# Kernel optimization log

Measured on AMD Instinct MI355X. Metric: run time of the kernel, lower is better.

The kernel has to match this reference:

```python
import jax, jax.numpy as jnp
import numpy as np

D = 256
H = 4
L = 6
N = 32768
NH = N // H  # 8192 per-head width
VOCAB = 256
B, T = 1, 1024
ROPE_BASE = 10000.0


def ln(x):
    # LayerNorm over last dim, no affine (elementwise_affine=False)
    m = jnp.mean(x, axis=-1, keepdims=True)
    v = jnp.var(x, axis=-1, keepdims=True)
    return (x - m) * jax.lax.rsqrt(v + 1e-5)


def rope(x):
    # standard rotary position embedding over the last dim (split-half convention)
    Dh = x.shape[-1]
    t = x.shape[-2]
    half = Dh // 2
    inv_freq = 1.0 / (ROPE_BASE ** (jnp.arange(half, dtype=jnp.float32) / half))
    ang = jnp.arange(t, dtype=jnp.float32)[:, None] * inv_freq[None, :]  # [T, half]
    cos, sin = jnp.cos(ang), jnp.sin(ang)
    x1, x2 = x[..., :half], x[..., half:]
    return jnp.concatenate([x1 * cos - x2 * sin, x2 * cos + x1 * sin], axis=-1)


def setup_inputs() -> dict:
    key = jax.random.key(0)
    ks = jax.random.split(key, 6)
    std = 0.02
    return {
        "idx": jax.random.randint(ks[0], (B, T), 0, VOCAB, dtype=jnp.int32),
        "wte": std * jax.random.normal(ks[1], (VOCAB, D), dtype=jnp.float32),
        "encoder": std * jax.random.normal(ks[2], (N, D), dtype=jnp.float32),
        "decoder_x": std * jax.random.normal(ks[3], (H, D, NH), dtype=jnp.float32),
        "decoder_y": std * jax.random.normal(ks[4], (H, D, NH), dtype=jnp.float32),
        "readout": std * jax.random.normal(ks[5], (D, VOCAB), dtype=jnp.float32),
    }


def reference(idx, wte, encoder, decoder_x, decoder_y, readout):
    b, t = idx.shape
    v = ln(wte[idx])  # [B, T, D]
    # strict causal mask (tril with diagonal=-1): position i attends to j < i
    mask = jnp.tril(jnp.ones((t, t), dtype=bool), k=-1)
    for _ in range(L):
        # x: relu(v @ decoder_x) -> [B, H, T, NH]
        x = jax.nn.relu(jnp.einsum('btd,hdn->bhtn', v, decoder_x))
        xr = rope(x)  # Q = K = x
        # unnormalized causal linear attention, strict lower triangular
        scores = jnp.einsum('bhtn,bhsn->bhts', xr, xr)
        scores = jnp.where(mask, scores, 0.0)
        a = jnp.einsum('bhts,bsd->bhtd', scores, v)  # V = v (broadcast over heads)
        # gated wide projection
        y = jax.nn.relu(jnp.einsum('bhtd,hdn->bhtn', ln(a), decoder_y)) * x
        # [B,H,T,NH] -> [B,T,H*NH] = [B,T,N]  (matches transpose(1,2).reshape)
        y = jnp.transpose(y, (0, 2, 1, 3)).reshape(b, t, N)
        v = ln(v + ln(y @ encoder))  # dropout is identity in eval
    return v @ readout  # [B, T, VOCAB]
```

## Files before the change

### kernel.cpp

```cpp
#include <hip/hip_runtime.h>
#include <hip/hip_bf16.h>
#include <stdint.h>

typedef unsigned short u16;
typedef unsigned int u32;
typedef __attribute__((ext_vector_type(8))) short i16x8;
typedef __attribute__((ext_vector_type(4))) float f32x4;

#define DEV __device__ __forceinline__

constexpr int T = 1024, D = 256, H = 4, NH = 8192, NF = 32768, HALF = 4096;

constexpr size_t OFF_DXT  = 0;
constexpr size_t OFF_DYT  = OFF_DXT  + (size_t)H*NH*D*2;
constexpr size_t OFF_ENCT = OFF_DYT  + (size_t)H*NH*D*2;
constexpr size_t OFF_ROT  = OFF_ENCT + (size_t)D*NF*2;
constexpr size_t OFF_COS  = OFF_ROT  + (size_t)D*D*2;
constexpr size_t OFF_SIN  = OFF_COS  + (size_t)T*HALF*4;
constexpr size_t OFF_V    = OFF_SIN  + (size_t)T*HALF*4;
constexpr size_t OFF_VBF  = OFF_V    + (size_t)T*D*4;
constexpr size_t OFF_VT   = OFF_VBF  + (size_t)T*D*2;
constexpr size_t OFF_X    = OFF_VT   + (size_t)T*D*2;
constexpr size_t OFF_XR   = OFF_X    + (size_t)T*NF*2;
constexpr size_t OFF_SC   = OFF_XR   + (size_t)T*NF*2;
constexpr size_t OFF_LA   = OFF_SC   + (size_t)H*T*T*2;
constexpr size_t OFF_PART = OFF_LA   + (size_t)H*T*D*2;
constexpr size_t WS_NEED  = OFF_PART + (size_t)8*T*T*4;


DEV u16 f2bf(float f) {
  u32 u = __float_as_uint(f);
  u += 0x7FFFu + ((u >> 16) & 1u);
  return (u16)(u >> 16);
}
DEV float bf2f(u16 u) { return __uint_as_float(((u32)u) << 16); }

DEV float2 block_sum2(float a, float b, float* sb) {
  #pragma unroll
  for (int o = 32; o > 0; o >>= 1) {
    a += __shfl_down(a, o, 64);
    b += __shfl_down(b, o, 64);
  }
  const int w = threadIdx.x >> 6;
  __syncthreads();
  if ((threadIdx.x & 63) == 0) { sb[w*2] = a; sb[w*2+1] = b; }
  __syncthreads();
  return make_float2(sb[0]+sb[2]+sb[4]+sb[6], sb[1]+sb[3]+sb[5]+sb[7]);
}

DEV void stage128(const u16* __restrict__ g, int ld, char* lds, int wave, int lane) {
  #pragma unroll
  for (int i = 0; i < 4; ++i) {
    const int f = (wave*4 + i)*64 + lane;
    const int row = f >> 3, seg = f & 7;
    const int segl = seg ^ (row & 7);
    const u16* src = g + (size_t)row*ld + segl*8;
    __builtin_amdgcn_global_load_lds(
        (const __attribute__((address_space(1))) void*)src,
        (__attribute__((address_space(3))) void*)(lds + ((wave*4 + i) << 10)),
        16, 0, 0);
  }
}

DEV void mfma_tile(const char* Ac, const char* Bc, int wm, int wn, int lr, int lk,
                   f32x4 acc[4][4]) {
  #pragma unroll
  for (int kk = 0; kk < 2; ++kk) {
    const int lcol = kk*64 + lk*16;
    i16x8 af[4], bfv[4];
    #pragma unroll
    for (int m = 0; m < 4; ++m) {
      const int row = wm*64 + m*16 + lr;
      af[m] = *(const i16x8*)(Ac + row*128 + (lcol ^ ((row & 7) << 4)));
    }
    #pragma unroll
    for (int n = 0; n < 4; ++n) {
      const int row = wn*64 + n*16 + lr;
      bfv[n] = *(const i16x8*)(Bc + row*128 + (lcol ^ ((row & 7) << 4)));
    }
    #pragma unroll
    for (int m = 0; m < 4; ++m)
      #pragma unroll
      for (int n = 0; n < 4; ++n)
        acc[m][n] = __builtin_amdgcn_mfma_f32_16x16x32_bf16(af[m], bfv[n], acc[m][n], 0, 0, 0);
  }
}

DEV void gemm_bt_core(const u16* __restrict__ Ab, int lda,
                      const u16* __restrict__ Bb, int ldb,
                      int nkt, char* smem, f32x4 acc[4][4]) {
  const int tid = threadIdx.x, lane = tid & 63, wave = tid >> 6;
  const int wm = wave >> 1, wn = wave & 1;
  const int lr = lane & 15, lk = lane >> 4;
  char* As = smem;
  char* Bs = smem + 32768;
  #pragma unroll
  for (int m = 0; m < 4; ++m)
    #pragma unroll
    for (int n = 0; n < 4; ++n) acc[m][n] = f32x4{0.f, 0.f, 0.f, 0.f};
  stage128(Ab, lda, As, wave, lane);
  stage128(Bb, ldb, Bs, wave, lane);
  __syncthreads();
  for (int kt = 0; kt < nkt; ++kt) {
    const int cur = kt & 1;
    if (kt + 1 < nkt) {
      stage128(Ab + (size_t)(kt+1)*64, lda, As + ((cur^1) << 14), wave, lane);
      stage128(Bb + (size_t)(kt+1)*64, ldb, Bs + ((cur^1) << 14), wave, lane);
    }
    mfma_tile(As + (cur << 14), Bs + (cur << 14), wm, wn, lr, lk, acc);
    __syncthreads();
  }
}

DEV void gemm_bt_core_sb(const u16* __restrict__ Ab, int lda,
                         const u16* __restrict__ Bb, int ldb,
                         int nkt, char* smem, f32x4 acc[4][4]) {
  const int tid = threadIdx.x, lane = tid & 63, wave = tid >> 6;
  const int wm = wave >> 1, wn = wave & 1;
  const int lr = lane & 15, lk = lane >> 4;
  char* As = smem;
  char* Bs = smem + 16384;
  #pragma unroll
  for (int m = 0; m < 4; ++m)
    #pragma unroll
    for (int n = 0; n < 4; ++n) acc[m][n] = f32x4{0.f, 0.f, 0.f, 0.f};
  for (int kt = 0; kt < nkt; ++kt) {
    stage128(Ab + (size_t)kt*64, lda, As, wave, lane);
    stage128(Bb + (size_t)kt*64, ldb, Bs, wave, lane);
    __syncthreads();
    mfma_tile(As, Bs, wm, wn, lr, lk, acc);
    __syncthreads();
  }
}

#define EPILOG_IDX() \
  const int lane = threadIdx.x & 63, wave = threadIdx.x >> 6; \
  const int wm = wave >> 1, wn = wave & 1, lr = lane & 15, lk = lane >> 4; \
  const int r0 = wm*64 + lk*4; \
  const int c0 = wn*64 + lr;

constexpr int TS = 136;

template<int MODE>
DEV void store_tile(const f32x4 acc[4][4], u16* __restrict__ dst, int ld,
                    const u16* __restrict__ xg, char* smem) {
  u16* tb = (u16*)smem;
  EPILOG_IDX();
  #pragma unroll
  for (int m = 0; m < 4; ++m)
    #pragma unroll
    for (int n = 0; n < 4; ++n)
      #pragma unroll
      for (int r = 0; r < 4; ++r) {
        float v = acc[m][n][r];
        if (MODE >= 1) v = fmaxf(v, 0.f);
        tb[(size_t)(r0 + m*16 + r)*TS + c0 + n*16] = f2bf(v);
      }
  __syncthreads();
  const int rr = threadIdx.x >> 4;
  const int cc = (threadIdx.x & 15)*8;
  #pragma unroll
  for (int it = 0; it < 8; ++it) {
    const int row = it*16 + rr;
    i16x8 w = *(const i16x8*)(tb + (size_t)row*TS + cc);
    if (MODE == 2) {
      const i16x8 xv = *(const i16x8*)(xg + (size_t)row*ld + cc);
      #pragma unroll
      for (int j = 0; j < 8; ++j)
        w[j] = (short)f2bf(bf2f((u16)w[j]) * bf2f((u16)xv[j]));
    }
    *(i16x8*)(dst + (size_t)row*ld + cc) = w;
  }
}

template<int MODE>
DEV void store_tile_sb(const f32x4 acc[4][4], u16* __restrict__ dst, int ld,
                       const u16* __restrict__ xg, char* smem) {
  u16* tb = (u16*)smem;
  const int lane = threadIdx.x & 63, wave = threadIdx.x >> 6;
  const int wm = wave >> 1, wn = wave & 1, lr = lane & 15, lk = lane >> 4;
  const int c0 = wn*64 + lr, rb = lk*4;
  const int rr = threadIdx.x >> 4, cc = (threadIdx.x & 15)*8;
  #pragma unroll
  for (int half = 0; half < 2; ++half) {
    if (wm == half) {
      #pragma unroll
      for (int m = 0; m < 4; ++m)
        #pragma unroll
        for (int n = 0; n < 4; ++n)
          #pragma unroll
          for (int r = 0; r < 4; ++r) {
            float v = acc[m][n][r];
            if (MODE >= 1) v = fmaxf(v, 0.f);
            tb[(size_t)(rb + m*16 + r)*TS + c0 + n*16] = f2bf(v);
          }
    }
    __syncthreads();
    #pragma unroll
    for (int it = 0; it < 4; ++it) {
      const int row = it*16 + rr;
      const int grow = half*64 + row;
      i16x8 w = *(const i16x8*)(tb + (size_t)row*TS + cc);
      if (MODE == 2) {
        const i16x8 xv = *(const i16x8*)(xg + (size_t)grow*ld + cc);
        #pragma unroll
        for (int j = 0; j < 8; ++j)
          w[j] = (short)f2bf(bf2f((u16)w[j]) * bf2f((u16)xv[j]));
      }
      *(i16x8*)(dst + (size_t)grow*ld + cc) = w;
    }
    __syncthreads();
  }
}

template<int PERM>
__global__ __launch_bounds__(256) void k_transpose_cvt(const float* __restrict__ in,
                                                       u16* __restrict__ out, int R, int C) {
  __shared__ float tile[32][33];
  const size_t zoff = (size_t)blockIdx.z * R * C;
  const float* inz = in + zoff;
  u16* outz = out + zoff;
  const int c0 = blockIdx.x << 5, rr0 = blockIdx.y << 5;
  const int tx = threadIdx.x & 31, ty = threadIdx.x >> 5;
  #pragma unroll
  for (int i = 0; i < 4; ++i) {
    int irow = rr0 + ty + i*8;
    if (PERM == 2) {
      const int hh = irow >> 13, j = irow & 8191;
      irow = hh*8192 + ((j & 1) ? (j >> 1) + 4096 : (j >> 1));
    }
    tile[ty + i*8][tx] = inz[(size_t)irow*C + c0 + tx];
  }
  __syncthreads();
  #pragma unroll
  for (int i = 0; i < 4; ++i) {
    const int rr = ty + i*8;
    int orow = c0 + rr;
    if (PERM == 1) {
      const int j = orow & 8191;
      orow = (orow & ~8191) | ((j < 4096) ? 2*j : 2*(j - 4096) + 1);
    }
    outz[(size_t)orow*R + rr0 + tx] = f2bf(tile[tx][rr]);
  }
}

__global__ __launch_bounds__(256) void k_rope_table(float* __restrict__ cosT,
                                                    float* __restrict__ sinT) {
  const int i = blockIdx.x*256 + threadIdx.x;
  const int t = blockIdx.y;
  const float p = (float)i * (1.f/4096.f);
  const float ang = (float)t * expf(-9.210340371976184f * p);
  cosT[(size_t)t*HALF + i] = cosf(ang);
  sinT[(size_t)t*HALF + i] = sinf(ang);
}

__global__ __launch_bounds__(256) void k_embed(const int* __restrict__ idx,
                                               const float* __restrict__ wte,
                                               float* __restrict__ v,
                                               u16* __restrict__ vbf, u16* __restrict__ vT) {
  __shared__ float sb[8];
  const int t = blockIdx.x, d = threadIdx.x;
  const float val = wte[(size_t)idx[t]*D + d];
  float2 ss = block_sum2(val, val*val, sb);
  const float m = ss.x*(1.f/256.f), var = ss.y*(1.f/256.f) - m*m;
  const float vn = (val - m) * rsqrtf(var + 1e-5f);
  v[(size_t)t*D + d] = vn;
  const u16 b = f2bf(vn);
  vbf[(size_t)t*D + d] = b;
  vT[(size_t)d*T + t] = b;
}

__global__ __launch_bounds__(256) void k_gemm_x_rope(const u16* __restrict__ vbf,
                                                     const u16* __restrict__ dxT,
                                                     u16* __restrict__ x,
                                                     u16* __restrict__ xr,
                                                     const float* __restrict__ cosT,
                                                     const float* __restrict__ sinT) {
  __shared__ char smem[32768];
  const int nt = blockIdx.x, mt = blockIdx.y, h = blockIdx.z;
  f32x4 acc[4][4];
  gemm_bt_core_sb(vbf + (size_t)mt*128*D, D,
                  dxT + ((size_t)h*NH + (size_t)nt*128)*D, D, 4, smem, acc);
  u16* tb = (u16*)smem;
  const int lane = threadIdx.x & 63, wave = threadIdx.x >> 6;
  const int wm = wave >> 1, wn = wave & 1, lr = lane & 15, lk = lane >> 4;
  const int c0 = wn*64 + lr, rb = lk*4;
  const int rr = threadIdx.x >> 4, cc = (threadIdx.x & 15)*8;
  const size_t obase = (size_t)mt*128*NF + (size_t)h*NH + (size_t)nt*128;
  const int pbase = (nt*128 + cc) >> 1;
  #pragma unroll
  for (int half = 0; half < 2; ++half) {
    if (wm == half) {
      #pragma unroll
      for (int m = 0; m < 4; ++m)
        #pragma unroll
        for (int n = 0; n < 4; ++n)
          #pragma unroll
          for (int r = 0; r < 4; ++r)
            tb[(size_t)(rb + m*16 + r)*TS + c0 + n*16] = f2bf(fmaxf(acc[m][n][r], 0.f));
    }
    __syncthreads();
    #pragma unroll
    for (int it = 0; it < 4; ++it) {
      const int row = it*16 + rr;
      const int grow = half*64 + row;
      const i16x8 w = *(const i16x8*)(tb + (size_t)row*TS + cc);
      *(i16x8*)(x + obase + (size_t)grow*NF + cc) = w;
      const int t = mt*128 + grow;
      const float4 cv = *(const float4*)(cosT + (size_t)t*HALF + pbase);
      const float4 sv = *(const float4*)(sinT + (size_t)t*HALF + pbase);
      i16x8 rg;
      float x1, x2;
      x1 = bf2f((u16)w[0]); x2 = bf2f((u16)w[1]);
      rg[0] = (short)f2bf(x1*cv.x - x2*sv.x); rg[1] = (short)f2bf(x2*cv.x + x1*sv.x);
      x1 = bf2f((u16)w[2]); x2 = bf2f((u16)w[3]);
      rg[2] = (short)f2bf(x1*cv.y - x2*sv.y); rg[3] = (short)f2bf(x2*cv.y + x1*sv.y);
      x1 = bf2f((u16)w[4]); x2 = bf2f((u16)w[5]);
      rg[4] = (short)f2bf(x1*cv.z - x2*sv.z); rg[5] = (short)f2bf(x2*cv.z + x1*sv.z);
      x1 = bf2f((u16)w[6]); x2 = bf2f((u16)w[7]);
      rg[6] = (short)f2bf(x1*cv.w - x2*sv.w); rg[7] = (short)f2bf(x2*cv.w + x1*sv.w);
      *(i16x8*)(xr + obase + (size_t)grow*NF + cc) = rg;
    }
    __syncthreads();
  }
}

__global__ __launch_bounds__(256) void k_gemm_sc(const u16* __restrict__ xr,
                                                 u16* __restrict__ scb) {
  __shared__ char smem[65536];
  const int z = blockIdx.x & 15;
  const int i = blockIdx.x >> 4;
  int tt = 0;
  while ((tt + 1)*(tt + 2)/2 <= i) ++tt;
  const int st = i - tt*(tt + 1)/2;
  const int h = z >> 2, kc = z & 3;
  const u16* base = xr + (size_t)h*NH + (size_t)kc*2048;
  f32x4 acc[4][4];
  gemm_bt_core(base + (size_t)tt*128*NF, NF, base + (size_t)st*128*NF, NF, 32, smem, acc);
  store_tile<0>(acc, scb + (size_t)z*T*T + (size_t)tt*128*T + (size_t)st*128, T,
                nullptr, smem);
}

__global__ __launch_bounds__(256) void k_sc_combine(const u16* __restrict__ scb,
                                                    u16* __restrict__ sc) {
  const int row = blockIdx.x;
  const int h = row >> 10, t = row & 1023;
  const u16* p0 = scb + ((size_t)(h*4 + 0)*T + t)*T;
  u16* o = sc + (size_t)row*T;
  const int s0 = threadIdx.x*4;
  ushort4 r;
  if (s0 >= t) {
    r.x = 0; r.y = 0; r.z = 0; r.w = 0;
  } else {
    const ushort4 a0 = *(const ushort4*)(p0 + s0);
    const ushort4 a1 = *(const ushort4*)(p0 + T*T + s0);
    const ushort4 a2 = *(const ushort4*)(p0 + 2*(size_t)T*T + s0);
    const ushort4 a3 = *(const ushort4*)(p0 + 3*(size_t)T*T + s0);
    const float vx = bf2f(a0.x) + bf2f(a1.x) + bf2f(a2.x) + bf2f(a3.x);
    const float vy = bf2f(a0.y) + bf2f(a1.y) + bf2f(a2.y) + bf2f(a3.y);
    const float vz = bf2f(a0.z) + bf2f(a1.z) + bf2f(a2.z) + bf2f(a3.z);
    const float vw = bf2f(a0.w) + bf2f(a1.w) + bf2f(a2.w) + bf2f(a3.w);
    r.x = f2bf((s0 + 0 < t) ? vx : 0.f);
    r.y = f2bf((s0 + 1 < t) ? vy : 0.f);
    r.z = f2bf((s0 + 2 < t) ? vz : 0.f);
    r.w = f2bf((s0 + 3 < t) ? vw : 0.f);
  }
  *(ushort4*)(o + s0) = r;
}

__global__ __launch_bounds__(256) void k_gemm_av(const u16* __restrict__ sc,
                                                 const u16* __restrict__ vT,
                                                 float* __restrict__ part) {
  __shared__ char smem[65536];
  const int slot = blockIdx.x & 7;
  const int h = slot >> 1, nt = slot & 1;
  int mt = 0, kc = 0, rem = blockIdx.x >> 3;
  #pragma unroll
  for (int m = 0; m < 8; ++m) {
    const int c = (m >> 1) + 1;
    if (rem < c) { mt = m; kc = rem; break; }
    rem -= c;
  }
  f32x4 acc[4][4];
  gemm_bt_core(sc + ((size_t)h*T + (size_t)mt*128)*T + (size_t)kc*256, T,
               vT + (size_t)nt*128*T + (size_t)kc*256, T, 4, smem, acc);
  EPILOG_IDX();
  float* Cp = part + (size_t)(h*4 + kc) * T * D;
  const int tb = mt*128 + r0, cb = nt*128 + c0;
  #pragma unroll
  for (int m = 0; m < 4; ++m)
    #pragma unroll
    for (int n = 0; n < 4; ++n)
      #pragma unroll
      for (int r = 0; r < 4; ++r)
        Cp[(size_t)(tb + m*16 + r)*D + cb + n*16] = acc[m][n][r];
}

__global__ __launch_bounds__(256) void k_ln_a(const float* __restrict__ part,
                                              u16* __restrict__ la) {
  __shared__ float sb[8];
  const int row = blockIdx.x;
  const int h = row >> 10, t = row & 1023;
  const int d = threadIdx.x;
  const int nkc = ((t >> 7) >> 1) + 1;
  float s = 0.f;
  for (int kc = 0; kc < nkc; ++kc)
    s += part[((size_t)(h*4 + kc)*T + t)*D + d];
  float2 ss = block_sum2(s, s*s, sb);
  const float m = ss.x*(1.f/256.f), var = ss.y*(1.f/256.f) - m*m;
  la[(size_t)row*D + d] = f2bf((s - m) * rsqrtf(var + 1e-5f));
}

__global__ __launch_bounds__(256) void k_gemm_y(const u16* __restrict__ la,
                                                const u16* __restrict__ dyT,
                                                const u16* __restrict__ x,
                                                u16* __restrict__ y) {
  __shared__ char smem[32768];
  const int nt = blockIdx.x, mt = blockIdx.y, h = blockIdx.z;
  f32x4 acc[4][4];
  gemm_bt_core_sb(la + ((size_t)h*T + (size_t)mt*128)*D, D,
                  dyT + ((size_t)h*NH + (size_t)nt*128)*D, D, 4, smem, acc);
  const size_t off = (size_t)mt*128*NF + (size_t)h*NH + (size_t)nt*128;
  store_tile_sb<2>(acc, y + off, NF, x + off, smem);
}

__global__ __launch_bounds__(256) void k_gemm_enc(const u16* __restrict__ y,
                                                  const u16* __restrict__ encT,
                                                  float* __restrict__ part) {
  __shared__ char smem[65536];
  const int slot = blockIdx.x & 7;
  const int seq  = blockIdx.x >> 3;
  const int kcc = slot*4 + (seq >> 4);
  const int nt = seq & 1;
  const int mt = (seq >> 1) & 7;
  f32x4 acc[4][4];
  gemm_bt_core(y + (size_t)mt*128*NF + (size_t)kcc*1024, NF,
               encT + (size_t)nt*128*NF + (size_t)kcc*1024, NF, 16, smem, acc);
  EPILOG_IDX();
  float* Cp = part + (size_t)kcc * T * D;
  const int tb = mt*128 + r0, cb = nt*128 + c0;
  #pragma unroll
  for (int m = 0; m < 4; ++m)
    #pragma unroll
    for (int n = 0; n < 4; ++n)
      #pragma unroll
      for (int r = 0; r < 4; ++r)
        Cp[(size_t)(tb + m*16 + r)*D + cb + n*16] = acc[m][n][r];
}

__global__ __launch_bounds__(256) void k_newv(const float* __restrict__ part,
                                              float* __restrict__ v,
                                              u16* __restrict__ vbf, u16* __restrict__ vT) {
  __shared__ float sb[8];
  const int t = blockIdx.x, d = threadIdx.x;
  float s = 0.f;
  #pragma unroll
  for (int kc = 0; kc < 32; ++kc)
    s += part[((size_t)kc*T + t)*D + d];
  float2 ss = block_sum2(s, s*s, sb);
  float m = ss.x*(1.f/256.f), var = ss.y*(1.f/256.f) - m*m;
  const float l1 = (s - m) * rsqrtf(var + 1e-5f);
  const float u = v[(size_t)t*D + d] + l1;
  float2 s2 = block_sum2(u, u*u, sb);
  m = s2.x*(1.f/256.f); var = s2.y*(1.f/256.f) - m*m;
  const float vn = (u - m) * rsqrtf(var + 1e-5f);
  v[(size_t)t*D + d] = vn;
  const u16 bb = f2bf(vn);
  vbf[(size_t)t*D + d] = bb;
  vT[(size_t)d*T + t] = bb;
}

__global__ __launch_bounds__(256) void k_gemm_out(const u16* __restrict__ vbf,
                                                  const u16* __restrict__ roT,
                                                  float* __restrict__ out) {
  __shared__ char smem[65536];
  const int nt = blockIdx.x, mt = blockIdx.y;
  f32x4 acc[4][4];
  gemm_bt_core(vbf + (size_t)mt*128*D, D, roT + (size_t)nt*128*D, D, 4, smem, acc);
  EPILOG_IDX();
  const int tb = mt*128 + r0, cb = nt*128 + c0;
  #pragma unroll
  for (int m = 0; m < 4; ++m)
    #pragma unroll
    for (int n = 0; n < 4; ++n)
      #pragma unroll
      for (int r = 0; r < 4; ++r)
        out[(size_t)(tb + m*16 + r)*D + cb + n*16] = acc[m][n][r];
}

extern "C" void kernel_launch(void* const* d_in, const int* in_sizes, int n_in,
                              void* d_out, int out_size, void* d_ws, size_t ws_size,
                              hipStream_t stream) {
  (void)in_sizes; (void)n_in; (void)out_size; (void)ws_size;
  const int*   idx = (const int*)d_in[0];
  const float* wte = (const float*)d_in[1];
  const float* enc = (const float*)d_in[2];
  const float* dx  = (const float*)d_in[3];
  const float* dy  = (const float*)d_in[4];
  const float* ro  = (const float*)d_in[5];
  float* out = (float*)d_out;
  char* ws = (char*)d_ws;

  u16* dxT  = (u16*)(ws + OFF_DXT);
  u16* dyT  = (u16*)(ws + OFF_DYT);
  u16* encT = (u16*)(ws + OFF_ENCT);
  u16* roT  = (u16*)(ws + OFF_ROT);
  float* cosT = (float*)(ws + OFF_COS);
  float* sinT = (float*)(ws + OFF_SIN);
  float* v    = (float*)(ws + OFF_V);
  u16* vbf  = (u16*)(ws + OFF_VBF);
  u16* vT   = (u16*)(ws + OFF_VT);
  u16* x    = (u16*)(ws + OFF_X);
  u16* xr   = (u16*)(ws + OFF_XR);
  u16* sc   = (u16*)(ws + OFF_SC);
  u16* la   = (u16*)(ws + OFF_LA);
  u16* scb  = (u16*)(ws + OFF_PART);
  float* part = (float*)(ws + OFF_PART);

  k_transpose_cvt<1><<<dim3(NH/32, D/32, H), 256, 0, stream>>>(dx, dxT, D, NH);
  k_transpose_cvt<1><<<dim3(NH/32, D/32, H), 256, 0, stream>>>(dy, dyT, D, NH);
  k_transpose_cvt<2><<<dim3(D/32, NF/32, 1), 256, 0, stream>>>(enc, encT, NF, D);
  k_transpose_cvt<0><<<dim3(D/32, D/32, 1), 256, 0, stream>>>(ro, roT, D, D);
  k_rope_table<<<dim3(HALF/256, T), 256, 0, stream>>>(cosT, sinT);
  k_embed<<<T, 256, 0, stream>>>(idx, wte, v, vbf, vT);

  for (int l = 0; l < 6; ++l) {
    k_gemm_x_rope<<<dim3(64, 8, H), 256, 0, stream>>>(vbf, dxT, x, xr, cosT, sinT);
    k_gemm_sc <<<576,              256, 0, stream>>>(xr, scb);
    k_sc_combine<<<H*T,            256, 0, stream>>>(scb, sc);
    k_gemm_av <<<160,              256, 0, stream>>>(sc, vT, part);
    k_ln_a    <<<H*T,              256, 0, stream>>>(part, la);
    k_gemm_y  <<<dim3(64, 8, H),   256, 0, stream>>>(la, dyT, x, xr );
    k_gemm_enc<<<512,              256, 0, stream>>>(xr , encT, part);
    k_newv    <<<T,                256, 0, stream>>>(part, v, vbf, vT);
  }
  k_gemm_out<<<dim3(2, 8), 256, 0, stream>>>(vbf, roT, out);
}
```

Before: 1.264 ms.

## Remap x-rope GEMM block order and use half-smem GEMM core for scores

Flattens the x-projection+RoPE GEMM grid into a 1D index whose block ordering is remapped to group tiles by head and N-slot. The intent is better L2 reuse of decoder weights and activations on the multi-XCD chip. The score GEMM switches to the 32KB shared-memory core and store path, which may allow higher occupancy. The risk is that the remap hurts locality if the ordering does not match how blocks are dispatched across XCDs.

```diff
diff --git a/kernel.cpp b/kernel.cpp
--- a/kernel.cpp
+++ b/kernel.cpp
@@ -142,38 +142,6 @@
 constexpr int TS = 136;
 
 template<int MODE>
-DEV void store_tile(const f32x4 acc[4][4], u16* __restrict__ dst, int ld,
-                    const u16* __restrict__ xg, char* smem) {
-  u16* tb = (u16*)smem;
-  EPILOG_IDX();
-  #pragma unroll
-  for (int m = 0; m < 4; ++m)
-    #pragma unroll
-    for (int n = 0; n < 4; ++n)
-      #pragma unroll
-      for (int r = 0; r < 4; ++r) {
-        float v = acc[m][n][r];
-        if (MODE >= 1) v = fmaxf(v, 0.f);
-        tb[(size_t)(r0 + m*16 + r)*TS + c0 + n*16] = f2bf(v);
-      }
-  __syncthreads();
-  const int rr = threadIdx.x >> 4;
-  const int cc = (threadIdx.x & 15)*8;
-  #pragma unroll
-  for (int it = 0; it < 8; ++it) {
-    const int row = it*16 + rr;
-    i16x8 w = *(const i16x8*)(tb + (size_t)row*TS + cc);
-    if (MODE == 2) {
-      const i16x8 xv = *(const i16x8*)(xg + (size_t)row*ld + cc);
-      #pragma unroll
-      for (int j = 0; j < 8; ++j)
-        w[j] = (short)f2bf(bf2f((u16)w[j]) * bf2f((u16)xv[j]));
-    }
-    *(i16x8*)(dst + (size_t)row*ld + cc) = w;
-  }
-}
-
-template<int MODE>
 DEV void store_tile_sb(const f32x4 acc[4][4], u16* __restrict__ dst, int ld,
                        const u16* __restrict__ xg, char* smem) {
   u16* tb = (u16*)smem;
@@ -277,7 +245,12 @@
                                                      const float* __restrict__ cosT,
                                                      const float* __restrict__ sinT) {
   __shared__ char smem[32768];
-  const int nt = blockIdx.x, mt = blockIdx.y, h = blockIdx.z;
+  const int p = blockIdx.x;
+  const int slot = p & 7;
+  const int h = (p >> 3) & 3;
+  const int seq = p >> 5;
+  const int nt = slot*8 + (seq & 7);
+  const int mt = seq >> 3;
   f32x4 acc[4][4];
   gemm_bt_core_sb(vbf + (size_t)mt*128*D, D,
                   dxT + ((size_t)h*NH + (size_t)nt*128)*D, D, 4, smem, acc);
@@ -327,7 +300,7 @@
 
 __global__ __launch_bounds__(256) void k_gemm_sc(const u16* __restrict__ xr,
                                                  u16* __restrict__ scb) {
-  __shared__ char smem[65536];
+  __shared__ char smem[32768];
   const int z = blockIdx.x & 15;
   const int i = blockIdx.x >> 4;
   int tt = 0;
@@ -336,9 +309,9 @@
   const int h = z >> 2, kc = z & 3;
   const u16* base = xr + (size_t)h*NH + (size_t)kc*2048;
   f32x4 acc[4][4];
-  gemm_bt_core(base + (size_t)tt*128*NF, NF, base + (size_t)st*128*NF, NF, 32, smem, acc);
-  store_tile<0>(acc, scb + (size_t)z*T*T + (size_t)tt*128*T + (size_t)st*128, T,
-                nullptr, smem);
+  gemm_bt_core_sb(base + (size_t)tt*128*NF, NF, base + (size_t)st*128*NF, NF, 32, smem, acc);
+  store_tile_sb<0>(acc, scb + (size_t)z*T*T + (size_t)tt*128*T + (size_t)st*128, T,
+                   nullptr, smem);
 }
 
 __global__ __launch_bounds__(256) void k_sc_combine(const u16* __restrict__ scb,
@@ -525,7 +498,7 @@
   k_embed<<<T, 256, 0, stream>>>(idx, wte, v, vbf, vT);
 
   for (int l = 0; l < 6; ++l) {
-    k_gemm_x_rope<<<dim3(64, 8, H), 256, 0, stream>>>(vbf, dxT, x, xr, cosT, sinT);
+    k_gemm_x_rope<<<2048,          256, 0, stream>>>(vbf, dxT, x, xr, cosT, sinT);
     k_gemm_sc <<<576,              256, 0, stream>>>(xr, scb);
     k_sc_combine<<<H*T,            256, 0, stream>>>(scb, sc);
     k_gemm_av <<<160,              256, 0, stream>>>(sc, vT, part);
```

After: 1.320 ms. +4.5%, slower.
